# Performance work log

Measured on AMD Instinct MI355X. Metric: run time of the kernel, lower is better.

## Reference

```python
import jax, jax.numpy as jnp
import numpy as np

# dims: B batch, C tokens-per-patch, S num_patches, T input_channel(=output_channel), D d_model, P pool_size
B, C, S, T, D, P = 8, 512, 64, 128, 256, 8
EPS = 1e-5


def _cos_attn(pooled, keys):
    # pooled: (B,S,F), keys: (P,F) -> softmax over pool of cosine similarities: (B,S,P)
    pn = pooled / (jnp.linalg.norm(pooled, axis=-1, keepdims=True) + 1e-8)
    kn = keys / (jnp.linalg.norm(keys, axis=-1, keepdims=True) + 1e-8)
    return jax.nn.softmax(jnp.einsum('bsf,pf->bsp', pn, kn), axis=-1)


def setup_inputs() -> dict:
    key = jax.random.key(0)
    ks = jax.random.split(key, 5)
    sc = lambda k, shape, fan: jax.random.normal(k, shape, jnp.float32) * np.float32(1.0 / np.sqrt(fan))
    return {
        'x': jax.random.normal(ks[0], (B, C, S, T), jnp.float32),
        'gamma': jnp.ones((T,), jnp.float32),
        'beta': jnp.zeros((T,), jnp.float32),
        'keys1': sc(ks[1], (P, T), T),      # routing keys, WeightPool1
        'Wp1': sc(ks[2], (P, D, T), T),     # weight bank, T -> D
        'bp1': jnp.zeros((P, D), jnp.float32),
        'keys2': sc(ks[3], (P, D), D),      # routing keys, WeightPool2
        'Wp2': sc(ks[4], (P, T, D), D),     # weight bank, D -> T
        'bp2': jnp.zeros((P, T), jnp.float32),
    }


def reference(x, gamma, beta, keys1, Wp1, bp1, keys2, Wp2, bp2):
    # x_proj = Identity(x) since input_channel == output_channel
    # BatchNorm2d over channel T (x permuted to (B,T,S,C)) == normalize x over dims (0,1,2)
    mean = x.mean(axis=(0, 1, 2))
    var = x.var(axis=(0, 1, 2))  # biased, as torch BN training stats
    y = (x - mean) * jax.lax.rsqrt(var + EPS) * gamma + beta  # (B,C,S,T)

    # WeightPool1: pool over C, cosine-route into weight bank
    a1 = _cos_attn(y.mean(axis=1), keys1)            # (B,S,P)
    w1 = jnp.einsum('bsp,pdt->bsdt', a1, Wp1)        # (B,S,D,T)
    b1 = jnp.einsum('bsp,pd->bsd', a1, bp1)          # (B,S,D)

    y = jnp.einsum('bcst,bsdt->bcsd', y, w1) + b1[:, None]  # (B,C,S,D)
    y = jax.nn.relu(y)
    # dropout: inference mode (identity)

    # WeightPool2
    a2 = _cos_attn(y.mean(axis=1), keys2)            # (B,S,P)
    w2 = jnp.einsum('bsp,ptd->bstd', a2, Wp2)        # (B,S,T,D)
    b2 = jnp.einsum('bsp,pt->bst', a2, bp2)          # (B,S,T)

    y = jnp.einsum('bcsd,bstd->bcst', y, w2) + b2[:, None]  # (B,C,S,T)
    return (x + y, w1, w2)
```

## Files before the change

kernel.cpp:

```cpp
#include <hip/hip_runtime.h>
#include <hip/hip_bf16.h>

#define BB 8
#define CC 512
#define SS 64
#define TT 128
#define DD 256
#define PP 8
#define BS (BB*SS)
#define NSTAT (BB*CC*SS)
#define EPSV 1e-5f

typedef float f32x4 __attribute__((ext_vector_type(4)));
typedef __bf16 bf16x8 __attribute__((ext_vector_type(8)));

__device__ __forceinline__ unsigned short f2bf(float f) {
  unsigned u = __float_as_uint(f);
  u += 0x7FFFu + ((u >> 16) & 1u);
  return (unsigned short)(u >> 16);
}
__device__ __forceinline__ float bf2f(unsigned short h) {
  return __uint_as_float(((unsigned)h) << 16);
}

__global__ __launch_bounds__(256) void k1_stats(const float* __restrict__ x,
    float* __restrict__ csum_part, float* __restrict__ ssq_part,
    unsigned short* __restrict__ xbf) {
  int bid = blockIdx.x;
  int bs = bid >> 2, cq = bid & 3;
  int b = bs >> 6, s = bs & 63;
  const float* xb = x + ((size_t)b * CC * SS + s) * TT;
  unsigned short* xo = xbf + ((size_t)b * CC * SS + s) * TT;
  int tid = threadIdx.x;
  int t4 = tid & 31, coff = tid >> 5;
  float cs0=0,cs1=0,cs2=0,cs3=0, ss0=0,ss1=0,ss2=0,ss3=0;
  #pragma unroll 8
  for (int k = 0; k < 16; k++) {
    int c = cq*128 + coff + k*8;
    float4 v = *reinterpret_cast<const float4*>(xb + (size_t)c*(SS*TT) + t4*4);
    ushort4 o; o.x=f2bf(v.x); o.y=f2bf(v.y); o.z=f2bf(v.z); o.w=f2bf(v.w);
    *reinterpret_cast<ushort4*>(xo + (size_t)c*(SS*TT) + t4*4) = o;
    cs0 += v.x; cs1 += v.y; cs2 += v.z; cs3 += v.w;
    ss0 += v.x*v.x; ss1 += v.y*v.y; ss2 += v.z*v.z; ss3 += v.w*v.w;
  }
  __shared__ float4 redC[256];
  __shared__ float4 redS[256];
  redC[tid] = make_float4(cs0,cs1,cs2,cs3);
  redS[tid] = make_float4(ss0,ss1,ss2,ss3);
  __syncthreads();
  if (tid < 32) {
    #pragma unroll
    for (int j = 1; j < 8; j++) {
      float4 a = redC[tid + j*32], bq = redS[tid + j*32];
      cs0+=a.x; cs1+=a.y; cs2+=a.z; cs3+=a.w;
      ss0+=bq.x; ss1+=bq.y; ss2+=bq.z; ss3+=bq.w;
    }
    int t0 = tid*4;
    csum_part[(size_t)(t0+0)*2048 + bid] = cs0;
    csum_part[(size_t)(t0+1)*2048 + bid] = cs1;
    csum_part[(size_t)(t0+2)*2048 + bid] = cs2;
    csum_part[(size_t)(t0+3)*2048 + bid] = cs3;
    ssq_part[(size_t)(t0+0)*2048 + bid] = ss0;
    ssq_part[(size_t)(t0+1)*2048 + bid] = ss1;
    ssq_part[(size_t)(t0+2)*2048 + bid] = ss2;
    ssq_part[(size_t)(t0+3)*2048 + bid] = ss3;
  }
}

__global__ __launch_bounds__(256) void k1b_reduce(
    const float* __restrict__ csum_part, const float* __restrict__ ssq_part,
    float* __restrict__ sumt, float* __restrict__ sumsq) {
  int t = blockIdx.x, tid = threadIdx.x;
  const float* cp = csum_part + (size_t)t*2048;
  const float* sp = ssq_part + (size_t)t*2048;
  float cs = 0.f, ss = 0.f;
  #pragma unroll
  for (int k=0;k<8;k++) { cs += cp[tid + k*256]; ss += sp[tid + k*256]; }
  #pragma unroll
  for (int off=32; off; off>>=1) { cs += __shfl_xor(cs,off); ss += __shfl_xor(ss,off); }
  __shared__ float redc[4], reds[4];
  int wave = tid >> 6, lane = tid & 63;
  if (lane == 0) { redc[wave] = cs; reds[wave] = ss; }
  __syncthreads();
  if (tid == 0) {
    sumt[t]  = redc[0]+redc[1]+redc[2]+redc[3];
    sumsq[t] = reds[0]+reds[1]+reds[2]+reds[3];
  }
}

__global__ __launch_bounds__(256) void k2_route1(
    const float* __restrict__ sumt, const float* __restrict__ sumsq,
    const float* __restrict__ csum_part, const float* __restrict__ gamma,
    const float* __restrict__ beta, const float* __restrict__ keys1,
    const float* __restrict__ Wp1, const float* __restrict__ bp1,
    float* __restrict__ w1out, unsigned short* __restrict__ w1bf,
    float* __restrict__ b1) {
  int bid = blockIdx.x;
  int bs = bid >> 2, q = bid & 3;
  int tid = threadIdx.x;
  __shared__ float a1s[PP];
  if (tid < 64) {
    float pv0, pv1;
    {
      int t = tid;
      float4 c4v = *reinterpret_cast<const float4*>(csum_part + (size_t)t*2048 + bs*4);
      float cs = c4v.x + c4v.y + c4v.z + c4v.w;
      float m = sumt[t] * (1.f/NSTAT);
      float var = sumsq[t]*(1.f/NSTAT) - m*m;
      float g = gamma[t] * rsqrtf(var + EPSV);
      pv0 = (cs*(1.f/CC) - m)*g + beta[t];
    }
    {
      int t = tid + 64;
      float4 c4v = *reinterpret_cast<const float4*>(csum_part + (size_t)t*2048 + bs*4);
      float cs = c4v.x + c4v.y + c4v.z + c4v.w;
      float m = sumt[t] * (1.f/NSTAT);
      float var = sumsq[t]*(1.f/NSTAT) - m*m;
      float g = gamma[t] * rsqrtf(var + EPSV);
      pv1 = (cs*(1.f/CC) - m)*g + beta[t];
    }
    float ssq = pv0*pv0 + pv1*pv1;
    #pragma unroll
    for (int off=32; off; off>>=1) ssq += __shfl_xor(ssq, off);
    float pn = sqrtf(ssq) + 1e-8f;
    float lg[PP];
    #pragma unroll
    for (int p=0;p<PP;p++) {
      float k0 = keys1[p*TT + tid], k1 = keys1[p*TT + tid + 64];
      float dot = pv0*k0 + pv1*k1;
      float kn = k0*k0 + k1*k1;
      #pragma unroll
      for (int off=32; off; off>>=1) { dot += __shfl_xor(dot,off); kn += __shfl_xor(kn,off); }
      lg[p] = dot / (pn * (sqrtf(kn) + 1e-8f));
    }
    if (tid == 0) {
      float mx = lg[0];
      #pragma unroll
      for (int p=1;p<PP;p++) mx = fmaxf(mx, lg[p]);
      float se = 0.f, e[PP];
      #pragma unroll
      for (int p=0;p<PP;p++){ e[p] = __expf(lg[p]-mx); se += e[p]; }
      float inv = 1.f/se;
      #pragma unroll
      for (int p=0;p<PP;p++) a1s[p] = e[p]*inv;
    }
  }
  __syncthreads();
  float a[PP];
  #pragma unroll
  for (int p=0;p<PP;p++) a[p]=a1s[p];
  #pragma unroll
  for (int i=0;i<8;i++) {
    int idx = tid + i*256;
    int dr = idx >> 5, c4 = idx & 31;
    size_t roff = (size_t)(q*64+dr)*TT + c4*4;
    size_t off = (size_t)bs*(DD*TT) + roff;
    float4 accv = make_float4(0.f,0.f,0.f,0.f);
    #pragma unroll
    for (int p=0;p<PP;p++) {
      float4 v = *reinterpret_cast<const float4*>(Wp1 + (size_t)p*(DD*TT) + roff);
      accv.x += a[p]*v.x; accv.y += a[p]*v.y; accv.z += a[p]*v.z; accv.w += a[p]*v.w;
    }
    *reinterpret_cast<float4*>(w1out + off) = accv;
    ushort4 o; o.x=f2bf(accv.x); o.y=f2bf(accv.y); o.z=f2bf(accv.z); o.w=f2bf(accv.w);
    *reinterpret_cast<ushort4*>(w1bf + off) = o;
  }
  if (tid < 64) {
    int d = q*64 + tid;
    float bacc = 0.f;
    #pragma unroll
    for (int p=0;p<PP;p++) bacc += a[p]*bp1[p*DD + d];
    b1[(size_t)bs*DD + d] = bacc;
  }
}

__global__ __launch_bounds__(512) void k3_gemm1(
    const unsigned short* __restrict__ xbf, const float* __restrict__ sumt,
    const float* __restrict__ sumsq, const float* __restrict__ gamma,
    const float* __restrict__ beta, const unsigned short* __restrict__ w1bf,
    const float* __restrict__ b1, unsigned short* __restrict__ zbf,
    float* __restrict__ p2part) {
  int bid = blockIdx.x;
  int bs = bid >> 2, mt = bid & 3;
  int b = bs >> 6, s = bs & 63;
  __shared__ unsigned short lA[128*128];
  __shared__ unsigned short lB[256*128];
  __shared__ float mean_s[TT], g_s[TT], beta_s[TT];
  int tid = threadIdx.x;
  if (tid < TT) {
    float m = sumt[tid]*(1.f/NSTAT);
    float var = sumsq[tid]*(1.f/NSTAT) - m*m;
    mean_s[tid] = m;
    g_s[tid] = gamma[tid]*rsqrtf(var+EPSV);
    beta_s[tid] = beta[tid];
  }
  __syncthreads();
  char* lAc = reinterpret_cast<char*>(lA);
  char* lBc = reinterpret_cast<char*>(lB);
  auto bn2 = [&](unsigned pair, int t0) -> unsigned {
    float lo = bf2f((unsigned short)(pair & 0xFFFFu));
    float hi = bf2f((unsigned short)(pair >> 16));
    lo = (lo - mean_s[t0])*g_s[t0] + beta_s[t0];
    hi = (hi - mean_s[t0+1])*g_s[t0+1] + beta_s[t0+1];
    return ((unsigned)f2bf(hi) << 16) | (unsigned)f2bf(lo);
  };
  const unsigned short* xb = xbf + (((size_t)b*CC + mt*128)*SS + s)*TT;
  #pragma unroll
  for (int i=0;i<4;i++) {
    int flat = tid + i*512;
    int r = flat >> 4, c8 = flat & 15;
    int t0 = c8*8;
    uint4 v = *reinterpret_cast<const uint4*>(xb + (size_t)r*(SS*TT) + t0);
    uint4 o;
    o.x = bn2(v.x, t0); o.y = bn2(v.y, t0+2); o.z = bn2(v.z, t0+4); o.w = bn2(v.w, t0+6);
    unsigned addr = (unsigned)(r*256) + (((unsigned)(c8*16)) ^ (((unsigned)(r&7))<<4));
    *reinterpret_cast<uint4*>(lAc + addr) = o;
  }
  const unsigned short* wsrc = w1bf + (size_t)bs*(DD*TT);
  #pragma unroll
  for (int i=0;i<8;i++) {
    int flat = tid + i*512;
    int n = flat >> 4, ch = flat & 15;
    uint4 v = *reinterpret_cast<const uint4*>(wsrc + (size_t)flat*8);
    unsigned addr = (unsigned)(n*256) + (((unsigned)(ch*16)) ^ (((unsigned)(n&7))<<4));
    *reinterpret_cast<uint4*>(lBc + addr) = v;
  }
  __syncthreads();
  int wave = tid >> 6, lane = tid & 63;
  int wm = wave >> 2, wn = wave & 3;
  int lr = lane & 15, kg = lane >> 4;
  f32x4 zero = {0.f,0.f,0.f,0.f};
  f32x4 acc[4][4];
  #pragma unroll
  for (int m=0;m<4;m++)
    #pragma unroll
    for (int n=0;n<4;n++) acc[m][n] = zero;
  #pragma unroll
  for (int k0=0;k0<128;k0+=32) {
    bf16x8 af[4], bfr[4];
    #pragma unroll
    for (int m=0;m<4;m++) {
      int row = wm*64 + m*16 + lr;
      unsigned addr = (unsigned)(row*256) + (((unsigned)(k0*2 + kg*16)) ^ (((unsigned)(row&7))<<4));
      af[m] = *reinterpret_cast<const bf16x8*>(lAc + addr);
    }
    #pragma unroll
    for (int n=0;n<4;n++) {
      int row = wn*64 + n*16 + lr;
      unsigned addr = (unsigned)(row*256) + (((unsigned)(k0*2 + kg*16)) ^ (((unsigned)(row&7))<<4));
      bfr[n] = *reinterpret_cast<const bf16x8*>(lBc + addr);
    }
    #pragma unroll
    for (int m=0;m<4;m++)
      #pragma unroll
      for (int n=0;n<4;n++)
        acc[m][n] = __builtin_amdgcn_mfma_f32_16x16x32_bf16(af[m], bfr[n], acc[m][n], 0, 0, 0);
  }
  const float* b1p = b1 + (size_t)bs*DD;
  float* p2p = p2part + (((size_t)bid*2) + wm)*DD;
  __syncthreads();
  #pragma unroll
  for (int n=0;n<4;n++) {
    int d = wn*64 + n*16 + lr;
    float bv = b1p[d];
    float csum = 0.f;
    #pragma unroll
    for (int m=0;m<4;m++) {
      int rbase = wm*64 + m*16 + kg*4;
      #pragma unroll
      for (int j=0;j<4;j++) {
        float v = fmaxf(acc[m][n][j] + bv, 0.f);
        lB[(rbase+j)*DD + d] = f2bf(v);
        csum += v;
      }
    }
    csum += __shfl_xor(csum, 16);
    csum += __shfl_xor(csum, 32);
    if (kg == 0) p2p[d] = csum;
  }
  __syncthreads();
  unsigned short* zb = zbf + (((size_t)b*CC + mt*128)*SS + s)*DD;
  #pragma unroll
  for (int i=0;i<8;i++) {
    int flat = tid + i*512;
    int r = flat >> 5, ch = flat & 31;
    uint4 v = *reinterpret_cast<const uint4*>(lBc + flat*16);
    *reinterpret_cast<uint4*>(zb + (size_t)r*(SS*DD) + ch*8) = v;
  }
}

__global__ __launch_bounds__(256) void k4_route2(
    const float* __restrict__ p2part, const float* __restrict__ keys2,
    const float* __restrict__ Wp2, const float* __restrict__ bp2,
    float* __restrict__ w2out, unsigned short* __restrict__ w2bf,
    float* __restrict__ b2) {
  int bid = blockIdx.x;
  int bs = bid >> 2, q = bid & 3;
  int tid = threadIdx.x;
  __shared__ float a2s[PP];
  if (tid < 64) {
    float pv[4]; float ssq = 0.f;
    #pragma unroll
    for (int j=0;j<4;j++) {
      int d = tid + 64*j;
      float s8 = 0.f;
      #pragma unroll
      for (int r=0;r<8;r++) s8 += p2part[((size_t)bs*8 + r)*DD + d];
      pv[j] = s8 * (1.f/CC);
      ssq += pv[j]*pv[j];
    }
    #pragma unroll
    for (int off=32; off; off>>=1) ssq += __shfl_xor(ssq, off);
    float pn = sqrtf(ssq) + 1e-8f;
    float lg[PP];
    #pragma unroll
    for (int p=0;p<PP;p++) {
      float dot = 0.f, kn = 0.f;
      #pragma unroll
      for (int j=0;j<4;j++) {
        int d = tid + 64*j;
        float kv = keys2[p*DD + d];
        dot += pv[j]*kv; kn += kv*kv;
      }
      #pragma unroll
      for (int off=32; off; off>>=1) { dot += __shfl_xor(dot,off); kn += __shfl_xor(kn,off); }
      lg[p] = dot / (pn * (sqrtf(kn)+1e-8f));
    }
    if (tid == 0) {
      float mx = lg[0];
      #pragma unroll
      for (int p=1;p<PP;p++) mx = fmaxf(mx,lg[p]);
      float se=0.f, e[PP];
      #pragma unroll
      for (int p=0;p<PP;p++){ e[p]=__expf(lg[p]-mx); se+=e[p]; }
      float inv = 1.f/se;
      #pragma unroll
      for (int p=0;p<PP;p++) a2s[p]=e[p]*inv;
    }
  }
  __syncthreads();
  float a[PP];
  #pragma unroll
  for (int p=0;p<PP;p++) a[p]=a2s[p];
  #pragma unroll
  for (int i=0;i<8;i++) {
    int idx = tid + i*256;
    int tr = idx >> 6, c4 = idx & 63;
    size_t roff = (size_t)(q*32+tr)*DD + c4*4;
    size_t off = (size_t)bs*(TT*DD) + roff;
    float4 accv = make_float4(0.f,0.f,0.f,0.f);
    #pragma unroll
    for (int p=0;p<PP;p++) {
      float4 v = *reinterpret_cast<const float4*>(Wp2 + (size_t)p*(TT*DD) + roff);
      accv.x += a[p]*v.x; accv.y += a[p]*v.y; accv.z += a[p]*v.z; accv.w += a[p]*v.w;
    }
    *reinterpret_cast<float4*>(w2out + off) = accv;
    ushort4 o; o.x=f2bf(accv.x); o.y=f2bf(accv.y); o.z=f2bf(accv.z); o.w=f2bf(accv.w);
    *reinterpret_cast<ushort4*>(w2bf + off) = o;
  }
  if (tid < 32) {
    int t = q*32 + tid;
    float bacc = 0.f;
    #pragma unroll
    for (int p=0;p<PP;p++) bacc += a[p]*bp2[p*TT + t];
    b2[(size_t)bs*TT + t] = bacc;
  }
}

__global__ __launch_bounds__(512) void k5_gemm2(
    const unsigned short* __restrict__ zbf, const unsigned short* __restrict__ w2bf,
    const float* __restrict__ b2, const unsigned short* __restrict__ xbf,
    float* __restrict__ out) {
  int bid = blockIdx.x;
  int bs = bid >> 2, mt = bid & 3;
  int b = bs >> 6, s = bs & 63;
  __shared__ unsigned short lA[128*256];
  __shared__ unsigned short lB[128*256];
  int tid = threadIdx.x;
  char* lAc = reinterpret_cast<char*>(lA);
  char* lBc = reinterpret_cast<char*>(lB);
  const unsigned short* za = zbf + (((size_t)b*CC + mt*128)*SS + s)*DD;
  #pragma unroll
  for (int i=0;i<8;i++) {
    int flat = tid + i*512;
    int r = flat >> 5, ch = flat & 31;
    uint4 v = *reinterpret_cast<const uint4*>(za + (size_t)r*(SS*DD) + ch*8);
    unsigned addr = (unsigned)(r*512) + (((unsigned)(ch*16)) ^ (((unsigned)(r&7))<<4));
    *reinterpret_cast<uint4*>(lAc + addr) = v;
  }
  const unsigned short* wsrc = w2bf + (size_t)bs*(TT*DD);
  #pragma unroll
  for (int i=0;i<8;i++) {
    int flat = tid + i*512;
    int r = flat >> 5, ch = flat & 31;
    uint4 v = *reinterpret_cast<const uint4*>(wsrc + (size_t)flat*8);
    unsigned addr = (unsigned)(r*512) + (((unsigned)(ch*16)) ^ (((unsigned)(r&7))<<4));
    *reinterpret_cast<uint4*>(lBc + addr) = v;
  }
  __syncthreads();
  int wave = tid >> 6, lane = tid & 63;
  int wm = wave >> 2, wn = wave & 3;
  int lr = lane & 15, kg = lane >> 4;
  f32x4 zero = {0.f,0.f,0.f,0.f};
  f32x4 acc[4][2];
  #pragma unroll
  for (int m=0;m<4;m++)
    #pragma unroll
    for (int n=0;n<2;n++) acc[m][n] = zero;
  #pragma unroll
  for (int k0=0;k0<256;k0+=32) {
    bf16x8 af[4], bfr[2];
    #pragma unroll
    for (int m=0;m<4;m++) {
      int row = wm*64 + m*16 + lr;
      unsigned addr = (unsigned)(row*512) + (((unsigned)(k0*2 + kg*16)) ^ (((unsigned)(row&7))<<4));
      af[m] = *reinterpret_cast<const bf16x8*>(lAc + addr);
    }
    #pragma unroll
    for (int n=0;n<2;n++) {
      int row = wn*32 + n*16 + lr;
      unsigned addr = (unsigned)(row*512) + (((unsigned)(k0*2 + kg*16)) ^ (((unsigned)(row&7))<<4));
      bfr[n] = *reinterpret_cast<const bf16x8*>(lBc + addr);
    }
    #pragma unroll
    for (int m=0;m<4;m++)
      #pragma unroll
      for (int n=0;n<2;n++)
        acc[m][n] = __builtin_amdgcn_mfma_f32_16x16x32_bf16(af[m], bfr[n], acc[m][n], 0, 0, 0);
  }
  const float* b2p = b2 + (size_t)bs*TT;
  const unsigned short* xb = xbf + (((size_t)b*CC + mt*128)*SS + s)*TT;
  float* ob = out + (((size_t)b*CC + mt*128)*SS + s)*TT;
  #pragma unroll
  for (int n=0;n<2;n++) {
    int t = wn*32 + n*16 + lr;
    float bv = b2p[t];
    #pragma unroll
    for (int m=0;m<4;m++) {
      int rbase = wm*64 + m*16 + kg*4;
      #pragma unroll
      for (int j=0;j<4;j++) {
        size_t off = (size_t)(rbase+j)*(SS*TT) + t;
        ob[off] = acc[m][n][j] + bv + bf2f(xb[off]);
      }
    }
  }
}

extern "C" void kernel_launch(void* const* d_in, const int* in_sizes, int n_in,
                              void* d_out, int out_size, void* d_ws, size_t ws_size,
                              hipStream_t stream) {
  (void)in_sizes; (void)n_in; (void)out_size; (void)ws_size;
  const float* x     = (const float*)d_in[0];
  const float* gamma = (const float*)d_in[1];
  const float* beta  = (const float*)d_in[2];
  const float* keys1 = (const float*)d_in[3];
  const float* Wp1   = (const float*)d_in[4];
  const float* bp1   = (const float*)d_in[5];
  const float* keys2 = (const float*)d_in[6];
  const float* Wp2   = (const float*)d_in[7];
  const float* bp2   = (const float*)d_in[8];
  float* out = (float*)d_out;
  char* ws = (char*)d_ws;

  float* sumt        = (float*)(ws + 0);
  float* sumsq       = (float*)(ws + 512);
  float* csum_part   = (float*)(ws + 1024);
  float* ssq_part    = (float*)(ws + 1049600);
  float* p2part      = (float*)(ws + 2098176);
  float* b1          = (float*)(ws + 6292480);
  float* b2          = (float*)(ws + 6816768);
  unsigned short* w1bf = (unsigned short*)(ws + 7078912);
  unsigned short* w2bf = (unsigned short*)(ws + 40633344);
  unsigned short* xbf  = (unsigned short*)(ws + 74187776);
  unsigned short* zbf  = (unsigned short*)(ws + 141296640);

  float* w1out = out + 33554432;
  float* w2out = out + 50331648;

  k1_stats  <<<BS*4, 256, 0, stream>>>(x, csum_part, ssq_part, xbf);
  k1b_reduce<<<TT,   256, 0, stream>>>(csum_part, ssq_part, sumt, sumsq);
  k2_route1 <<<BS*4, 256, 0, stream>>>(sumt, sumsq, csum_part, gamma, beta, keys1, Wp1, bp1,
                                       w1out, w1bf, b1);
  k3_gemm1  <<<BS*4, 512, 0, stream>>>(xbf, sumt, sumsq, gamma, beta, w1bf, b1, zbf, p2part);
  k4_route2 <<<BS*4, 256, 0, stream>>>(p2part, keys2, Wp2, bp2, w2out, w2bf, b2);
  k5_gemm2  <<<BS*4, 512, 0, stream>>>(zbf, w2bf, b2, xbf, out);
}
```

Baseline: 291.0 us.

## Split GEMM1 over D halves and stage GEMM2 K in two halves to raise occupancy

GEMM1 now runs twice as many blocks, each computing half of the D columns, which halves the B tile in LDS, the accumulator registers and the LDS output staging (now swizzled). GEMM2 cuts its LDS footprint in half by splitting K=256 into two 128 chunks, loading the second chunk into registers while the first is multiplied. Both kernels get a min-blocks launch bound of 4. The aim is more resident blocks per CU and overlap of global loads with MFMA work. The cost is extra syncs, re-reading the A tile and row statistics in GEMM1, and register pressure from the prefetch buffers.

```diff
diff --git a/kernel.cpp b/kernel.cpp
--- a/kernel.cpp
+++ b/kernel.cpp
@@ -174,17 +174,18 @@
   }
 }
 
-__global__ __launch_bounds__(512) void k3_gemm1(
+__global__ __launch_bounds__(512, 4) void k3_gemm1(
     const unsigned short* __restrict__ xbf, const float* __restrict__ sumt,
     const float* __restrict__ sumsq, const float* __restrict__ gamma,
     const float* __restrict__ beta, const unsigned short* __restrict__ w1bf,
     const float* __restrict__ b1, unsigned short* __restrict__ zbf,
     float* __restrict__ p2part) {
   int bid = blockIdx.x;
-  int bs = bid >> 2, mt = bid & 3;
+  int bs = bid >> 3, sub = bid & 7;
+  int mt = sub >> 1, nh = sub & 1;
   int b = bs >> 6, s = bs & 63;
   __shared__ unsigned short lA[128*128];
-  __shared__ unsigned short lB[256*128];
+  __shared__ unsigned short lB[128*128];
   __shared__ float mean_s[TT], g_s[TT], beta_s[TT];
   int tid = threadIdx.x;
   if (tid < TT) {
@@ -218,10 +219,10 @@
   }
   const unsigned short* wsrc = w1bf + (size_t)bs*(DD*TT);
   #pragma unroll
-  for (int i=0;i<8;i++) {
+  for (int i=0;i<4;i++) {
     int flat = tid + i*512;
     int n = flat >> 4, ch = flat & 15;
-    uint4 v = *reinterpret_cast<const uint4*>(wsrc + (size_t)flat*8);
+    uint4 v = *reinterpret_cast<const uint4*>(wsrc + ((size_t)nh*2048 + flat)*8);
     unsigned addr = (unsigned)(n*256) + (((unsigned)(ch*16)) ^ (((unsigned)(n&7))<<4));
     *reinterpret_cast<uint4*>(lBc + addr) = v;
   }
@@ -230,14 +231,14 @@
   int wm = wave >> 2, wn = wave & 3;
   int lr = lane & 15, kg = lane >> 4;
   f32x4 zero = {0.f,0.f,0.f,0.f};
-  f32x4 acc[4][4];
+  f32x4 acc[4][2];
   #pragma unroll
   for (int m=0;m<4;m++)
     #pragma unroll
-    for (int n=0;n<4;n++) acc[m][n] = zero;
+    for (int n=0;n<2;n++) acc[m][n] = zero;
   #pragma unroll
   for (int k0=0;k0<128;k0+=32) {
-    bf16x8 af[4], bfr[4];
+    bf16x8 af[4], bfr[2];
     #pragma unroll
     for (int m=0;m<4;m++) {
       int row = wm*64 + m*16 + lr;
@@ -245,24 +246,25 @@
       af[m] = *reinterpret_cast<const bf16x8*>(lAc + addr);
     }
     #pragma unroll
-    for (int n=0;n<4;n++) {
-      int row = wn*64 + n*16 + lr;
+    for (int n=0;n<2;n++) {
+      int row = wn*32 + n*16 + lr;
       unsigned addr = (unsigned)(row*256) + (((unsigned)(k0*2 + kg*16)) ^ (((unsigned)(row&7))<<4));
       bfr[n] = *reinterpret_cast<const bf16x8*>(lBc + addr);
     }
     #pragma unroll
     for (int m=0;m<4;m++)
       #pragma unroll
-      for (int n=0;n<4;n++)
+      for (int n=0;n<2;n++)
         acc[m][n] = __builtin_amdgcn_mfma_f32_16x16x32_bf16(af[m], bfr[n], acc[m][n], 0, 0, 0);
   }
   const float* b1p = b1 + (size_t)bs*DD;
-  float* p2p = p2part + (((size_t)bid*2) + wm)*DD;
-  __syncthreads();
-  #pragma unroll
-  for (int n=0;n<4;n++) {
-    int d = wn*64 + n*16 + lr;
-    float bv = b1p[d];
+  float* p2row = p2part + (((size_t)(bs*4+mt)*2) + wm)*DD;
+  __syncthreads();
+  #pragma unroll
+  for (int n=0;n<2;n++) {
+    int dl = wn*32 + n*16 + lr;
+    int dg = nh*128 + dl;
+    float bv = b1p[dg];
     float csum = 0.f;
     #pragma unroll
     for (int m=0;m<4;m++) {
@@ -270,21 +272,24 @@
       #pragma unroll
       for (int j=0;j<4;j++) {
         float v = fmaxf(acc[m][n][j] + bv, 0.f);
-        lB[(rbase+j)*DD + d] = f2bf(v);
+        int row = rbase + j;
+        unsigned addr = (unsigned)(row*256) + (((unsigned)(dl*2)) ^ (((unsigned)(row&7))<<4));
+        *reinterpret_cast<unsigned short*>(lBc + addr) = f2bf(v);
         csum += v;
       }
     }
     csum += __shfl_xor(csum, 16);
     csum += __shfl_xor(csum, 32);
-    if (kg == 0) p2p[d] = csum;
-  }
-  __syncthreads();
-  unsigned short* zb = zbf + (((size_t)b*CC + mt*128)*SS + s)*DD;
-  #pragma unroll
-  for (int i=0;i<8;i++) {
-    int flat = tid + i*512;
-    int r = flat >> 5, ch = flat & 31;
-    uint4 v = *reinterpret_cast<const uint4*>(lBc + flat*16);
+    if (kg == 0) p2row[dg] = csum;
+  }
+  __syncthreads();
+  unsigned short* zb = zbf + (((size_t)b*CC + mt*128)*SS + s)*DD + nh*128;
+  #pragma unroll
+  for (int i=0;i<4;i++) {
+    int flat = tid + i*512;
+    int r = flat >> 4, ch = flat & 15;
+    unsigned addr = (unsigned)(r*256) + (((unsigned)(ch*16)) ^ (((unsigned)(r&7))<<4));
+    uint4 v = *reinterpret_cast<const uint4*>(lBc + addr);
     *reinterpret_cast<uint4*>(zb + (size_t)r*(SS*DD) + ch*8) = v;
   }
 }
@@ -367,37 +372,46 @@
   }
 }
 
-__global__ __launch_bounds__(512) void k5_gemm2(
+__global__ __launch_bounds__(512, 4) void k5_gemm2(
     const unsigned short* __restrict__ zbf, const unsigned short* __restrict__ w2bf,
     const float* __restrict__ b2, const unsigned short* __restrict__ xbf,
     float* __restrict__ out) {
   int bid = blockIdx.x;
   int bs = bid >> 2, mt = bid & 3;
   int b = bs >> 6, s = bs & 63;
-  __shared__ unsigned short lA[128*256];
-  __shared__ unsigned short lB[128*256];
+  __shared__ unsigned short lA[128*128];
+  __shared__ unsigned short lB[128*128];
   int tid = threadIdx.x;
   char* lAc = reinterpret_cast<char*>(lA);
   char* lBc = reinterpret_cast<char*>(lB);
   const unsigned short* za = zbf + (((size_t)b*CC + mt*128)*SS + s)*DD;
-  #pragma unroll
-  for (int i=0;i<8;i++) {
-    int flat = tid + i*512;
-    int r = flat >> 5, ch = flat & 31;
-    uint4 v = *reinterpret_cast<const uint4*>(za + (size_t)r*(SS*DD) + ch*8);
-    unsigned addr = (unsigned)(r*512) + (((unsigned)(ch*16)) ^ (((unsigned)(r&7))<<4));
-    *reinterpret_cast<uint4*>(lAc + addr) = v;
-  }
   const unsigned short* wsrc = w2bf + (size_t)bs*(TT*DD);
-  #pragma unroll
-  for (int i=0;i<8;i++) {
-    int flat = tid + i*512;
-    int r = flat >> 5, ch = flat & 31;
-    uint4 v = *reinterpret_cast<const uint4*>(wsrc + (size_t)flat*8);
-    unsigned addr = (unsigned)(r*512) + (((unsigned)(ch*16)) ^ (((unsigned)(r&7))<<4));
-    *reinterpret_cast<uint4*>(lBc + addr) = v;
-  }
-  __syncthreads();
+  int r0 = tid >> 4, ch0 = tid & 15;
+  uint4 ta[4], tb[4];
+  #pragma unroll
+  for (int i=0;i<4;i++) {
+    int flat = tid + i*512;
+    int r = flat >> 4, ch = flat & 15;
+    ta[i] = *reinterpret_cast<const uint4*>(za + (size_t)r*(SS*DD) + ch*8);
+    tb[i] = *reinterpret_cast<const uint4*>(wsrc + (size_t)r*DD + ch*8);
+  }
+  #pragma unroll
+  for (int i=0;i<4;i++) {
+    int flat = tid + i*512;
+    int r = flat >> 4, ch = flat & 15;
+    unsigned addr = (unsigned)(r*256) + (((unsigned)(ch*16)) ^ (((unsigned)(r&7))<<4));
+    *reinterpret_cast<uint4*>(lAc + addr) = ta[i];
+    *reinterpret_cast<uint4*>(lBc + addr) = tb[i];
+  }
+  __syncthreads();
+  uint4 ta2[4], tb2[4];
+  #pragma unroll
+  for (int i=0;i<4;i++) {
+    int flat = tid + i*512;
+    int r = flat >> 4, ch = flat & 15;
+    ta2[i] = *reinterpret_cast<const uint4*>(za + (size_t)r*(SS*DD) + 128 + ch*8);
+    tb2[i] = *reinterpret_cast<const uint4*>(wsrc + (size_t)r*DD + 128 + ch*8);
+  }
   int wave = tid >> 6, lane = tid & 63;
   int wm = wave >> 2, wn = wave & 3;
   int lr = lane & 15, kg = lane >> 4;
@@ -408,18 +422,18 @@
     #pragma unroll
     for (int n=0;n<2;n++) acc[m][n] = zero;
   #pragma unroll
-  for (int k0=0;k0<256;k0+=32) {
+  for (int k0=0;k0<128;k0+=32) {
     bf16x8 af[4], bfr[2];
     #pragma unroll
     for (int m=0;m<4;m++) {
       int row = wm*64 + m*16 + lr;
-      unsigned addr = (unsigned)(row*512) + (((unsigned)(k0*2 + kg*16)) ^ (((unsigned)(row&7))<<4));
+      unsigned addr = (unsigned)(row*256) + (((unsigned)(k0*2 + kg*16)) ^ (((unsigned)(row&7))<<4));
       af[m] = *reinterpret_cast<const bf16x8*>(lAc + addr);
     }
     #pragma unroll
     for (int n=0;n<2;n++) {
       int row = wn*32 + n*16 + lr;
-      unsigned addr = (unsigned)(row*512) + (((unsigned)(k0*2 + kg*16)) ^ (((unsigned)(row&7))<<4));
+      unsigned addr = (unsigned)(row*256) + (((unsigned)(k0*2 + kg*16)) ^ (((unsigned)(row&7))<<4));
       bfr[n] = *reinterpret_cast<const bf16x8*>(lBc + addr);
     }
     #pragma unroll
@@ -428,6 +442,38 @@
       for (int n=0;n<2;n++)
         acc[m][n] = __builtin_amdgcn_mfma_f32_16x16x32_bf16(af[m], bfr[n], acc[m][n], 0, 0, 0);
   }
+  __syncthreads();
+  #pragma unroll
+  for (int i=0;i<4;i++) {
+    int flat = tid + i*512;
+    int r = flat >> 4, ch = flat & 15;
+    unsigned addr = (unsigned)(r*256) + (((unsigned)(ch*16)) ^ (((unsigned)(r&7))<<4));
+    *reinterpret_cast<uint4*>(lAc + addr) = ta2[i];
+    *reinterpret_cast<uint4*>(lBc + addr) = tb2[i];
+  }
+  __syncthreads();
+  #pragma unroll
+  for (int k0=0;k0<128;k0+=32) {
+    bf16x8 af[4], bfr[2];
+    #pragma unroll
+    for (int m=0;m<4;m++) {
+      int row = wm*64 + m*16 + lr;
+      unsigned addr = (unsigned)(row*256) + (((unsigned)(k0*2 + kg*16)) ^ (((unsigned)(row&7))<<4));
+      af[m] = *reinterpret_cast<const bf16x8*>(lAc + addr);
+    }
+    #pragma unroll
+    for (int n=0;n<2;n++) {
+      int row = wn*32 + n*16 + lr;
+      unsigned addr = (unsigned)(row*256) + (((unsigned)(k0*2 + kg*16)) ^ (((unsigned)(row&7))<<4));
+      bfr[n] = *reinterpret_cast<const bf16x8*>(lBc + addr);
+    }
+    #pragma unroll
+    for (int m=0;m<4;m++)
+      #pragma unroll
+      for (int n=0;n<2;n++)
+        acc[m][n] = __builtin_amdgcn_mfma_f32_16x16x32_bf16(af[m], bfr[n], acc[m][n], 0, 0, 0);
+  }
+  (void)r0; (void)ch0;
   const float* b2p = b2 + (size_t)bs*TT;
   const unsigned short* xb = xbf + (((size_t)b*CC + mt*128)*SS + s)*TT;
   float* ob = out + (((size_t)b*CC + mt*128)*SS + s)*TT;
@@ -482,7 +528,7 @@
   k1b_reduce<<<TT,   256, 0, stream>>>(csum_part, ssq_part, sumt, sumsq);
   k2_route1 <<<BS*4, 256, 0, stream>>>(sumt, sumsq, csum_part, gamma, beta, keys1, Wp1, bp1,
                                        w1out, w1bf, b1);
-  k3_gemm1  <<<BS*4, 512, 0, stream>>>(xbf, sumt, sumsq, gamma, beta, w1bf, b1, zbf, p2part);
+  k3_gemm1  <<<BS*8, 512, 0, stream>>>(xbf, sumt, sumsq, gamma, beta, w1bf, b1, zbf, p2part);
   k4_route2 <<<BS*4, 256, 0, stream>>>(p2part, keys2, Wp2, bp2, w2out, w2bf, b2);
   k5_gemm2  <<<BS*4, 512, 0, stream>>>(zbf, w2bf, b2, xbf, out);
 }
```

Result: slower. 340.6 us (+17.1%).

## Fold batchnorm affine into routed w1 and bias; widen gemm2 blocks

Applied to the files above, without the earlier changes.

The per-channel batchnorm scale is folded into the bf16 copy of w1, and the shift term is folded into b1 through a dot product with the mixed weights. This lets gemm1 load raw bf16 x straight into LDS without per-element normalization math. Separately, gemm2 now runs 1024 threads per block, so each wave owns a smaller tile. The fold changes rounding, because gamma*rsqrt is applied before the bf16 conversion, and the larger block changes register and occupancy behaviour.

```diff
diff --git a/kernel.cpp b/kernel.cpp
--- a/kernel.cpp
+++ b/kernel.cpp
@@ -99,6 +99,15 @@
   int bs = bid >> 2, q = bid & 3;
   int tid = threadIdx.x;
   __shared__ float a1s[PP];
+  __shared__ float g_s[TT], h_s[TT];
+  __shared__ float db_s[64];
+  if (tid < TT) {
+    float m = sumt[tid] * (1.f/NSTAT);
+    float var = sumsq[tid]*(1.f/NSTAT) - m*m;
+    float g = gamma[tid] * rsqrtf(var + EPSV);
+    g_s[tid] = g;
+    h_s[tid] = beta[tid] - m*g;
+  }
   if (tid < 64) {
     float pv0, pv1;
     {
@@ -162,12 +171,21 @@
       accv.x += a[p]*v.x; accv.y += a[p]*v.y; accv.z += a[p]*v.z; accv.w += a[p]*v.w;
     }
     *reinterpret_cast<float4*>(w1out + off) = accv;
-    ushort4 o; o.x=f2bf(accv.x); o.y=f2bf(accv.y); o.z=f2bf(accv.z); o.w=f2bf(accv.w);
+    float4 gv = *reinterpret_cast<const float4*>(g_s + c4*4);
+    ushort4 o;
+    o.x=f2bf(accv.x*gv.x); o.y=f2bf(accv.y*gv.y);
+    o.z=f2bf(accv.z*gv.z); o.w=f2bf(accv.w*gv.w);
     *reinterpret_cast<ushort4*>(w1bf + off) = o;
-  }
+    float4 hv = *reinterpret_cast<const float4*>(h_s + c4*4);
+    float pd = accv.x*hv.x + accv.y*hv.y + accv.z*hv.z + accv.w*hv.w;
+    #pragma unroll
+    for (int off2=16; off2; off2>>=1) pd += __shfl_xor(pd, off2);
+    if (c4 == 0) db_s[dr] = pd;
+  }
+  __syncthreads();
   if (tid < 64) {
     int d = q*64 + tid;
-    float bacc = 0.f;
+    float bacc = db_s[tid];
     #pragma unroll
     for (int p=0;p<PP;p++) bacc += a[p]*bp1[p*DD + d];
     b1[(size_t)bs*DD + d] = bacc;
@@ -175,9 +193,7 @@
 }
 
 __global__ __launch_bounds__(512) void k3_gemm1(
-    const unsigned short* __restrict__ xbf, const float* __restrict__ sumt,
-    const float* __restrict__ sumsq, const float* __restrict__ gamma,
-    const float* __restrict__ beta, const unsigned short* __restrict__ w1bf,
+    const unsigned short* __restrict__ xbf, const unsigned short* __restrict__ w1bf,
     const float* __restrict__ b1, unsigned short* __restrict__ zbf,
     float* __restrict__ p2part) {
   int bid = blockIdx.x;
@@ -185,36 +201,17 @@
   int b = bs >> 6, s = bs & 63;
   __shared__ unsigned short lA[128*128];
   __shared__ unsigned short lB[256*128];
-  __shared__ float mean_s[TT], g_s[TT], beta_s[TT];
   int tid = threadIdx.x;
-  if (tid < TT) {
-    float m = sumt[tid]*(1.f/NSTAT);
-    float var = sumsq[tid]*(1.f/NSTAT) - m*m;
-    mean_s[tid] = m;
-    g_s[tid] = gamma[tid]*rsqrtf(var+EPSV);
-    beta_s[tid] = beta[tid];
-  }
-  __syncthreads();
   char* lAc = reinterpret_cast<char*>(lA);
   char* lBc = reinterpret_cast<char*>(lB);
-  auto bn2 = [&](unsigned pair, int t0) -> unsigned {
-    float lo = bf2f((unsigned short)(pair & 0xFFFFu));
-    float hi = bf2f((unsigned short)(pair >> 16));
-    lo = (lo - mean_s[t0])*g_s[t0] + beta_s[t0];
-    hi = (hi - mean_s[t0+1])*g_s[t0+1] + beta_s[t0+1];
-    return ((unsigned)f2bf(hi) << 16) | (unsigned)f2bf(lo);
-  };
   const unsigned short* xb = xbf + (((size_t)b*CC + mt*128)*SS + s)*TT;
   #pragma unroll
   for (int i=0;i<4;i++) {
     int flat = tid + i*512;
     int r = flat >> 4, c8 = flat & 15;
-    int t0 = c8*8;
-    uint4 v = *reinterpret_cast<const uint4*>(xb + (size_t)r*(SS*TT) + t0);
-    uint4 o;
-    o.x = bn2(v.x, t0); o.y = bn2(v.y, t0+2); o.z = bn2(v.z, t0+4); o.w = bn2(v.w, t0+6);
+    uint4 v = *reinterpret_cast<const uint4*>(xb + (size_t)r*(SS*TT) + c8*8);
     unsigned addr = (unsigned)(r*256) + (((unsigned)(c8*16)) ^ (((unsigned)(r&7))<<4));
-    *reinterpret_cast<uint4*>(lAc + addr) = o;
+    *reinterpret_cast<uint4*>(lAc + addr) = v;
   }
   const unsigned short* wsrc = w1bf + (size_t)bs*(DD*TT);
   #pragma unroll
@@ -367,7 +364,7 @@
   }
 }
 
-__global__ __launch_bounds__(512) void k5_gemm2(
+__global__ __launch_bounds__(1024, 4) void k5_gemm2(
     const unsigned short* __restrict__ zbf, const unsigned short* __restrict__ w2bf,
     const float* __restrict__ b2, const unsigned short* __restrict__ xbf,
     float* __restrict__ out) {
@@ -381,8 +378,8 @@
   char* lBc = reinterpret_cast<char*>(lB);
   const unsigned short* za = zbf + (((size_t)b*CC + mt*128)*SS + s)*DD;
   #pragma unroll
-  for (int i=0;i<8;i++) {
-    int flat = tid + i*512;
+  for (int i=0;i<4;i++) {
+    int flat = tid + i*1024;
     int r = flat >> 5, ch = flat & 31;
     uint4 v = *reinterpret_cast<const uint4*>(za + (size_t)r*(SS*DD) + ch*8);
     unsigned addr = (unsigned)(r*512) + (((unsigned)(ch*16)) ^ (((unsigned)(r&7))<<4));
@@ -390,8 +387,8 @@
   }
   const unsigned short* wsrc = w2bf + (size_t)bs*(TT*DD);
   #pragma unroll
-  for (int i=0;i<8;i++) {
-    int flat = tid + i*512;
+  for (int i=0;i<4;i++) {
+    int flat = tid + i*1024;
     int r = flat >> 5, ch = flat & 31;
     uint4 v = *reinterpret_cast<const uint4*>(wsrc + (size_t)flat*8);
     unsigned addr = (unsigned)(r*512) + (((unsigned)(ch*16)) ^ (((unsigned)(r&7))<<4));
@@ -402,17 +399,17 @@
   int wm = wave >> 2, wn = wave & 3;
   int lr = lane & 15, kg = lane >> 4;
   f32x4 zero = {0.f,0.f,0.f,0.f};
-  f32x4 acc[4][2];
-  #pragma unroll
-  for (int m=0;m<4;m++)
+  f32x4 acc[2][2];
+  #pragma unroll
+  for (int m=0;m<2;m++)
     #pragma unroll
     for (int n=0;n<2;n++) acc[m][n] = zero;
   #pragma unroll
   for (int k0=0;k0<256;k0+=32) {
-    bf16x8 af[4], bfr[2];
-    #pragma unroll
-    for (int m=0;m<4;m++) {
-      int row = wm*64 + m*16 + lr;
+    bf16x8 af[2], bfr[2];
+    #pragma unroll
+    for (int m=0;m<2;m++) {
+      int row = wm*32 + m*16 + lr;
       unsigned addr = (unsigned)(row*512) + (((unsigned)(k0*2 + kg*16)) ^ (((unsigned)(row&7))<<4));
       af[m] = *reinterpret_cast<const bf16x8*>(lAc + addr);
     }
@@ -423,7 +420,7 @@
       bfr[n] = *reinterpret_cast<const bf16x8*>(lBc + addr);
     }
     #pragma unroll
-    for (int m=0;m<4;m++)
+    for (int m=0;m<2;m++)
       #pragma unroll
       for (int n=0;n<2;n++)
         acc[m][n] = __builtin_amdgcn_mfma_f32_16x16x32_bf16(af[m], bfr[n], acc[m][n], 0, 0, 0);
@@ -436,8 +433,8 @@
     int t = wn*32 + n*16 + lr;
     float bv = b2p[t];
     #pragma unroll
-    for (int m=0;m<4;m++) {
-      int rbase = wm*64 + m*16 + kg*4;
+    for (int m=0;m<2;m++) {
+      int rbase = wm*32 + m*16 + kg*4;
       #pragma unroll
       for (int j=0;j<4;j++) {
         size_t off = (size_t)(rbase+j)*(SS*TT) + t;
@@ -478,11 +475,11 @@
   float* w1out = out + 33554432;
   float* w2out = out + 50331648;
 
-  k1_stats  <<<BS*4, 256, 0, stream>>>(x, csum_part, ssq_part, xbf);
-  k1b_reduce<<<TT,   256, 0, stream>>>(csum_part, ssq_part, sumt, sumsq);
-  k2_route1 <<<BS*4, 256, 0, stream>>>(sumt, sumsq, csum_part, gamma, beta, keys1, Wp1, bp1,
-                                       w1out, w1bf, b1);
-  k3_gemm1  <<<BS*4, 512, 0, stream>>>(xbf, sumt, sumsq, gamma, beta, w1bf, b1, zbf, p2part);
-  k4_route2 <<<BS*4, 256, 0, stream>>>(p2part, keys2, Wp2, bp2, w2out, w2bf, b2);
-  k5_gemm2  <<<BS*4, 512, 0, stream>>>(zbf, w2bf, b2, xbf, out);
-}
+  k1_stats  <<<BS*4, 256,  0, stream>>>(x, csum_part, ssq_part, xbf);
+  k1b_reduce<<<TT,   256,  0, stream>>>(csum_part, ssq_part, sumt, sumsq);
+  k2_route1 <<<BS*4, 256,  0, stream>>>(sumt, sumsq, csum_part, gamma, beta, keys1, Wp1, bp1,
+                                        w1out, w1bf, b1);
+  k3_gemm1  <<<BS*4, 512,  0, stream>>>(xbf, w1bf, b1, zbf, p2part);
+  k4_route2 <<<BS*4, 256,  0, stream>>>(p2part, keys2, Wp2, bp2, w2out, w2bf, b2);
+  k5_gemm2  <<<BS*4, 1024, 0, stream>>>(zbf, w2bf, b2, xbf, out);
+}
```

After: 293.9 us. About the same (+1.0%).
